# Kernel tuning notes

Hardware: AMD Instinct MI355X
Metric: run time of the kernel (lower is better)

The kernel has to match this reference:

```python
import jax, jax.numpy as jnp
import numpy as np

B, L, D = 64, 1024, 1024
NUM_CLASS = 126
C = NUM_CLASS + 2           # total tags incl. START/STOP
START, STOP = C - 2, C - 1


def setup_inputs() -> dict:
    key = jax.random.key(0)
    kx, kl, kw, kt, ky = jax.random.split(key, 5)
    x = jax.random.normal(kx, (B, L, D), dtype=jnp.float32)
    lengths = jax.random.randint(kl, (B,), L // 2, L + 1)
    mask = jnp.arange(L)[None, :] < lengths[:, None]          # prefix bool mask [B,L]
    y = jax.random.randint(ky, (B, L), 0, NUM_CLASS)
    W = jax.random.normal(kw, (D, C), dtype=jnp.float32) * 0.02
    b = jnp.zeros((C,), dtype=jnp.float32)
    transitions = jax.random.normal(kt, (C, C), dtype=jnp.float32)
    transitions = transitions.at[START, :].set(-1.0)
    transitions = transitions.at[:, STOP].set(-1.0)
    return {"x": x, "mask": mask, "y": y, "W": W, "b": b, "transitions": transitions}


def reference(x, mask, y, W, b, transitions):
    # fc (dropout is identity at eval time)
    emis = x @ W + b                                  # [B,L,C]
    seq_len = mask.sum(-1)                            # [B]

    # ---- Viterbi forward scan over time ----
    def step(scores, inp):
        e_l, m_l = inp                                # [B,C], [B]
        ns = scores[:, :, None] + transitions[None]   # [B,C_prev,C_cur]
        bp = jnp.argmax(ns, axis=1)                   # [B,C]
        new = jnp.max(ns, axis=1) + e_l
        scores = jnp.where(m_l[:, None], new, scores)
        return scores, bp

    scores0 = jnp.zeros((x.shape[0], C), dtype=emis.dtype)
    final, bps = jax.lax.scan(step, scores0, (emis.transpose(1, 0, 2), mask.T))
    final = final + transitions[:, STOP][None, :]
    last_tag = jnp.argmax(final, axis=-1)             # [B]

    # ---- vectorized backtracking (reverse scan) ----
    def bstep(cur, inp):
        bp_l, l = inp                                 # [B,C], scalar
        emit = jnp.where(l <= seq_len - 1, cur, 0)    # pad with 0 past seq end
        prev = jnp.take_along_axis(bp_l, cur[:, None], axis=1)[:, 0]
        upd = (l >= 1) & (l <= seq_len - 1)
        return jnp.where(upd, prev, cur), emit

    ls = jnp.arange(L - 1, -1, -1)
    _, path_rev = jax.lax.scan(bstep, last_tag, (bps[::-1], ls))
    best_paths = path_rev[::-1].T                     # [B,L] int
    return best_paths
```

## Files before the change

### kernel.cpp

```cpp
#include <hip/hip_runtime.h>
#include <stdint.h>

#define BB 64
#define LL 1024
#define DD 1024
#define CC 128
#define STOPTAG 127

__global__ __launch_bounds__(256) void k_emis(const float* __restrict__ x,
                                              const float* __restrict__ W,
                                              const float* __restrict__ bias,
                                              float* __restrict__ emis) {
    __shared__ float a_t[32][132];
    const int tid = threadIdx.x;
    const int bm  = blockIdx.x;
    const float* A = x + (size_t)bm * 128 * DD;
    const int tx = tid & 15, ty = tid >> 4;
    const int r0 = ty * 8, c0 = tx * 8;

    float acc[8][8];
#pragma unroll
    for (int i = 0; i < 8; ++i)
#pragma unroll
        for (int j = 0; j < 8; ++j) acc[i][j] = 0.0f;

    for (int kc = 0; kc < 32; ++kc) {
        __syncthreads();
#pragma unroll
        for (int i = 0; i < 4; ++i) {
            int s   = tid + 256 * i;
            int row = s >> 3;
            int k0  = (s & 7) * 4;
            float4 v = *(const float4*)(A + (size_t)row * DD + kc * 32 + k0);
            a_t[k0 + 0][row] = v.x;
            a_t[k0 + 1][row] = v.y;
            a_t[k0 + 2][row] = v.z;
            a_t[k0 + 3][row] = v.w;
        }
        __syncthreads();
        const float* Wp = W + (size_t)kc * 32 * CC;
#pragma unroll
        for (int k = 0; k < 32; ++k) {
            float4 w0 = *(const float4*)(Wp + k * CC + c0);
            float4 w1 = *(const float4*)(Wp + k * CC + c0 + 4);
            float4 pa = *(const float4*)&a_t[k][r0];
            float4 pb = *(const float4*)&a_t[k][r0 + 4];
            float av[8] = {pa.x, pa.y, pa.z, pa.w, pb.x, pb.y, pb.z, pb.w};
            float wv[8] = {w0.x, w0.y, w0.z, w0.w, w1.x, w1.y, w1.z, w1.w};
#pragma unroll
            for (int i = 0; i < 8; ++i)
#pragma unroll
                for (int j = 0; j < 8; ++j)
                    acc[i][j] = fmaf(av[i], wv[j], acc[i][j]);
        }
    }
    float4 bv0 = *(const float4*)(bias + c0);
    float4 bv1 = *(const float4*)(bias + c0 + 4);
    float bb[8] = {bv0.x, bv0.y, bv0.z, bv0.w, bv1.x, bv1.y, bv1.z, bv1.w};
#pragma unroll
    for (int i = 0; i < 8; ++i) {
        size_t row = (size_t)bm * 128 + r0 + i;
        float4 o0 = make_float4(acc[i][0] + bb[0], acc[i][1] + bb[1],
                                acc[i][2] + bb[2], acc[i][3] + bb[3]);
        float4 o1 = make_float4(acc[i][4] + bb[4], acc[i][5] + bb[5],
                                acc[i][6] + bb[6], acc[i][7] + bb[7]);
        *(float4*)(emis + row * CC + c0)     = o0;
        *(float4*)(emis + row * CC + c0 + 4) = o1;
    }
}


__global__ __launch_bounds__(512) void k_forward(float* __restrict__ emis,
                                                 const unsigned char* __restrict__ mask,
                                                 const float* __restrict__ T) {
    const int b    = blockIdx.x;
    const int tid  = threadIdx.x;
    const int w    = tid >> 6;
    const int lane = tid & 63;

    __shared__ float part[2][8][CC];
    __shared__ int s_len;
    if (tid == 0) s_len = 0;
    __syncthreads();

    if (tid < 256) {
        const bool is_b8 = (mask[1] != 0);
        int c;
        if (is_b8) {
            const uchar4* m4 = (const uchar4*)(mask + (size_t)b * LL);
            uchar4 mv = m4[tid];
            c = (mv.x != 0) + (mv.y != 0) + (mv.z != 0) + (mv.w != 0);
        } else {
            const int4* m4 = (const int4*)((const int*)(const void*)mask + (size_t)b * LL);
            int4 mv = m4[tid];
            c = (mv.x != 0) + (mv.y != 0) + (mv.z != 0) + (mv.w != 0);
        }
        atomicAdd(&s_len, c);
    }
    __syncthreads();
    const int len = s_len;

    float t0[16], t1[16];
#pragma unroll
    for (int j = 0; j < 16; ++j) {
        t0[j] = T[(size_t)(w * 16 + j) * CC + lane];
        t1[j] = T[(size_t)(w * 16 + j) * CC + lane + 64];
    }

    const int cc_fin = w * 16 + (lane & 15);
    float* eb = emis + (size_t)b * LL * CC;

    float s_val = 0.0f;
    float e_cur = eb[cc_fin];
    float e_n1  = eb[CC + cc_fin];

    for (int l = 0; l < len; ++l) {
        int lp = l + 2 < len ? l + 2 : len - 1;
        float e_n2 = eb[(size_t)lp * CC + cc_fin];

        float acc0 = -INFINITY, acc1 = -INFINITY;
#pragma unroll
        for (int jj = 0; jj < 8; ++jj) {
            float sa = __int_as_float(__builtin_amdgcn_readlane(__float_as_int(s_val), 2 * jj));
            float sb = __int_as_float(__builtin_amdgcn_readlane(__float_as_int(s_val), 2 * jj + 1));
            acc0 = fmaxf(fmaxf(sa + t0[2 * jj], sb + t0[2 * jj + 1]), acc0);
            acc1 = fmaxf(fmaxf(sa + t1[2 * jj], sb + t1[2 * jj + 1]), acc1);
        }
        int p = l & 1;
        part[p][w][lane]      = acc0;
        part[p][w][lane + 64] = acc1;
        asm volatile("s_waitcnt lgkmcnt(0)" ::: "memory");
        __builtin_amdgcn_s_barrier();
        float m0 = fmaxf(part[p][0][cc_fin], part[p][1][cc_fin]);
        float m1 = fmaxf(part[p][2][cc_fin], part[p][3][cc_fin]);
        float m2 = fmaxf(part[p][4][cc_fin], part[p][5][cc_fin]);
        float m3 = fmaxf(part[p][6][cc_fin], part[p][7][cc_fin]);
        float mx = fmaxf(fmaxf(m0, m1), fmaxf(m2, m3));
        s_val = mx + e_cur;
        eb[(size_t)l * CC + cc_fin] = s_val;
        e_cur = e_n1;
        e_n1  = e_n2;
    }
}

__device__ __forceinline__ unsigned mono_u32(float f) {
    unsigned u = __float_as_uint(f);
    return u ^ (unsigned)(((int)u >> 31) | 0x80000000);
}

__device__ __forceinline__ unsigned dpp_max64(unsigned m) {
    unsigned t;
    t = (unsigned)__builtin_amdgcn_update_dpp(0, (int)m, 0x111, 0xF, 0xF, true); m = m > t ? m : t;
    t = (unsigned)__builtin_amdgcn_update_dpp(0, (int)m, 0x112, 0xF, 0xF, true); m = m > t ? m : t;
    t = (unsigned)__builtin_amdgcn_update_dpp(0, (int)m, 0x114, 0xF, 0xF, true); m = m > t ? m : t;
    t = (unsigned)__builtin_amdgcn_update_dpp(0, (int)m, 0x118, 0xF, 0xF, true); m = m > t ? m : t;
    t = (unsigned)__builtin_amdgcn_update_dpp(0, (int)m, 0x142, 0xF, 0xF, true); m = m > t ? m : t;
    t = (unsigned)__builtin_amdgcn_update_dpp(0, (int)m, 0x143, 0xF, 0xF, true); m = m > t ? m : t;
    return m;
}

__device__ __forceinline__ int astep(float sA, float sB, int row,
                                     const float* ldsT, int lane) {
    int q = (row & 7) << 2;
    float c0 = sA + ldsT[row * CC + (lane ^ q)];
    float c1 = sB + ldsT[row * CC + ((lane ^ q) + 64)];
    unsigned m0 = mono_u32(c0), m1 = mono_u32(c1);
    unsigned m = m0 > m1 ? m0 : m1;
    m = dpp_max64(m);
    unsigned mx = (unsigned)__builtin_amdgcn_readlane((int)m, 63);
    unsigned long long bl0 = __ballot(m0 == mx);
    unsigned long long bl1 = __ballot(m1 == mx);
    return bl0 ? __builtin_ctzll(bl0) : (64 + __builtin_ctzll(bl1));
}

__global__ __launch_bounds__(64) void k_back(const float* __restrict__ slog,
                                             const unsigned char* __restrict__ mask,
                                             const float* __restrict__ T,
                                             int* __restrict__ out) {
    const int b    = blockIdx.x;
    const int lane = threadIdx.x;
    __shared__ float ldsT[CC * CC];

    {
        int q = (lane & 7) << 2;
        for (int r = 0; r < CC; ++r) {
            float v0 = T[(size_t)r * CC + lane];
            float v1 = T[(size_t)r * CC + lane + 64];
            ldsT[lane * CC + (r ^ q)]        = v0;
            ldsT[(lane + 64) * CC + (r ^ q)] = v1;
        }
    }
    int len = 0;
    {
        const bool is_b8 = (mask[1] != 0);
        if (is_b8) {
            const unsigned char* mrow = mask + (size_t)b * LL;
            for (int i = 0; i < 16; ++i)
                len += (int)__popcll(__ballot(mrow[lane + i * 64] != 0));
        } else {
            const int* mrow = (const int*)(const void*)mask + (size_t)b * LL;
            for (int i = 0; i < 16; ++i)
                len += (int)__popcll(__ballot(mrow[lane + i * 64] != 0));
        }
    }
    __syncthreads();

    const float* sb = slog + (size_t)b * LL * CC;
    int* ob         = out + (size_t)b * LL;

    for (int l = len + lane; l < LL; l += 64) ob[l] = 0;

    float f0 = sb[(size_t)(len - 1) * CC + lane];
    float f1 = sb[(size_t)(len - 1) * CC + lane + 64];
    int cur = astep(f0, f1, STOPTAG, ldsT, lane);
    if (lane == 0) ob[len - 1] = cur;

    int r = len - 2;
    float a0 = sb[(size_t)r * CC + lane];
    float a1 = sb[(size_t)r * CC + lane + 64];
    float b0 = sb[(size_t)(r - 1) * CC + lane];
    float b1 = sb[(size_t)(r - 1) * CC + lane + 64];
    while (r >= 2) {
        int rc = r - 2;
        int rd = r - 3 >= 0 ? r - 3 : 0;
        float n0 = sb[(size_t)rc * CC + lane];
        float n1 = sb[(size_t)rc * CC + lane + 64];
        float p0 = sb[(size_t)rd * CC + lane];
        float p1 = sb[(size_t)rd * CC + lane + 64];
        cur = astep(a0, a1, cur, ldsT, lane);
        if (lane == 0) ob[r] = cur;
        cur = astep(b0, b1, cur, ldsT, lane);
        if (lane == 0) ob[r - 1] = cur;
        a0 = n0; a1 = n1; b0 = p0; b1 = p1;
        r -= 2;
    }
    if (r == 1) {
        cur = astep(a0, a1, cur, ldsT, lane);
        if (lane == 0) ob[1] = cur;
        cur = astep(b0, b1, cur, ldsT, lane);
        if (lane == 0) ob[0] = cur;
    } else if (r == 0) {
        cur = astep(a0, a1, cur, ldsT, lane);
        if (lane == 0) ob[0] = cur;
    }
}

extern "C" void kernel_launch(void* const* d_in, const int* in_sizes, int n_in,
                              void* d_out, int out_size, void* d_ws, size_t ws_size,
                              hipStream_t stream) {
    (void)in_sizes; (void)n_in; (void)out_size; (void)ws_size;
    const float* x    = (const float*)d_in[0];
    const unsigned char* mask = (const unsigned char*)d_in[1];
    const float* W    = (const float*)d_in[3];
    const float* bias = (const float*)d_in[4];
    const float* T    = (const float*)d_in[5];
    int* out = (int*)d_out;

    float* emis = (float*)d_ws;

    k_emis<<<dim3(512), dim3(256), 0, stream>>>(x, W, bias, emis);
    k_forward<<<dim3(BB), dim3(512), 0, stream>>>(emis, mask, T);
    k_back<<<dim3(BB), dim3(64), 0, stream>>>(emis, mask, T, out);
}
```

Before: 1.296 ms.

## Stage emissions and scores through LDS in 16-step chunks in Viterbi forward

The forward scan now prefetches emission rows into double-buffered LDS chunks of 16 timesteps using coalesced float4 loads. Scores are buffered in LDS and written back to global memory a chunk at a time, replacing the per-step scalar global loads and stores. The partial-max buffer is transposed so each thread reads its 8 wave partials as two float4 LDS loads. The cost is extra LDS use and an extra barrier every 16 steps, and the chunk bookkeeping near the sequence end is intricate.

```diff
diff --git a/kernel.cpp b/kernel.cpp
--- a/kernel.cpp
+++ b/kernel.cpp
@@ -69,7 +69,6 @@
     }
 }
 
-
 __global__ __launch_bounds__(512) void k_forward(float* __restrict__ emis,
                                                  const unsigned char* __restrict__ mask,
                                                  const float* __restrict__ T) {
@@ -77,8 +76,12 @@
     const int tid  = threadIdx.x;
     const int w    = tid >> 6;
     const int lane = tid & 63;
-
-    __shared__ float part[2][8][CC];
+    const int trow = tid >> 5;
+    const int tcol = (tid & 31) * 4;
+
+    __shared__ __align__(16) float part[2][CC][12];
+    __shared__ __align__(16) float ldsE[2][16][CC];
+    __shared__ __align__(16) float ldsS[2][16][CC];
     __shared__ int s_len;
     if (tid == 0) s_len = 0;
     __syncthreads();
@@ -110,13 +113,31 @@
     const int cc_fin = w * 16 + (lane & 15);
     float* eb = emis + (size_t)b * LL * CC;
 
+    float4 rs;
+    {
+        float4 c0v = *(const float4*)(eb + (size_t)trow * CC + tcol);
+        float4 c1v = *(const float4*)(eb + (size_t)(16 + trow) * CC + tcol);
+        *(float4*)&ldsE[0][trow][tcol] = c0v;
+        *(float4*)&ldsE[1][trow][tcol] = c1v;
+        rs = *(const float4*)(eb + (size_t)(32 + trow) * CC + tcol);
+    }
+    __syncthreads();
+
     float s_val = 0.0f;
-    float e_cur = eb[cc_fin];
-    float e_n1  = eb[CC + cc_fin];
 
     for (int l = 0; l < len; ++l) {
-        int lp = l + 2 < len ? l + 2 : len - 1;
-        float e_n2 = eb[(size_t)lp * CC + cc_fin];
+        if ((l & 15) == 0 && l > 0) {
+            const int c = l >> 4;
+            asm volatile("s_waitcnt lgkmcnt(0)" ::: "memory");
+            __builtin_amdgcn_s_barrier();
+            asm volatile("" ::: "memory");
+            float4 v = *(const float4*)&ldsS[(c - 1) & 1][trow][tcol];
+            *(float4*)(eb + (size_t)(16 * (c - 1) + trow) * CC + tcol) = v;
+            *(float4*)&ldsE[(c + 1) & 1][trow][tcol] = rs;
+            int g = 16 * (c + 2) + trow;
+            g = g < len ? g : len - 1;
+            rs = *(const float4*)(eb + (size_t)g * CC + tcol);
+        }
 
         float acc0 = -INFINITY, acc1 = -INFINITY;
 #pragma unroll
@@ -126,20 +147,29 @@
             acc0 = fmaxf(fmaxf(sa + t0[2 * jj], sb + t0[2 * jj + 1]), acc0);
             acc1 = fmaxf(fmaxf(sa + t1[2 * jj], sb + t1[2 * jj + 1]), acc1);
         }
-        int p = l & 1;
-        part[p][w][lane]      = acc0;
-        part[p][w][lane + 64] = acc1;
+        const int p = l & 1;
+        part[p][lane][w]      = acc0;
+        part[p][lane + 64][w] = acc1;
         asm volatile("s_waitcnt lgkmcnt(0)" ::: "memory");
         __builtin_amdgcn_s_barrier();
-        float m0 = fmaxf(part[p][0][cc_fin], part[p][1][cc_fin]);
-        float m1 = fmaxf(part[p][2][cc_fin], part[p][3][cc_fin]);
-        float m2 = fmaxf(part[p][4][cc_fin], part[p][5][cc_fin]);
-        float m3 = fmaxf(part[p][6][cc_fin], part[p][7][cc_fin]);
-        float mx = fmaxf(fmaxf(m0, m1), fmaxf(m2, m3));
-        s_val = mx + e_cur;
-        eb[(size_t)l * CC + cc_fin] = s_val;
-        e_cur = e_n1;
-        e_n1  = e_n2;
+        asm volatile("" ::: "memory");
+
+        float4 q0 = *(const float4*)&part[p][cc_fin][0];
+        float4 q1 = *(const float4*)&part[p][cc_fin][4];
+        float m01 = fmaxf(q0.x, q0.y), m23 = fmaxf(q0.z, q0.w);
+        float m45 = fmaxf(q1.x, q1.y), m67 = fmaxf(q1.z, q1.w);
+        float mx  = fmaxf(fmaxf(m01, m23), fmaxf(m45, m67));
+        s_val = mx + ldsE[(l >> 4) & 1][l & 15][cc_fin];
+        if (lane < 16) ldsS[(l >> 4) & 1][l & 15][cc_fin] = s_val;
+    }
+
+    asm volatile("s_waitcnt lgkmcnt(0)" ::: "memory");
+    __syncthreads();
+    {
+        const int cf = (len - 1) >> 4;
+        float4 v = *(const float4*)&ldsS[cf & 1][trow][tcol];
+        int g = 16 * cf + trow;
+        if (g < len) *(float4*)(eb + (size_t)g * CC + tcol) = v;
     }
 }
 
```

After: 1.345 ms. 1.04x slower.

## Double-buffer emission GEMM LDS tiles and deepen backtrack prefetch pipeline

Applied to the files above, without the earlier changes.

The emission GEMM now uses two LDS buffers and prefetches the next K-chunk of x into registers while computing on the current one, cutting one barrier per iteration. The backtrack kernel issues loads for the first seven score rows before staging the transition matrix into LDS, and keeps a deeper rolling prefetch of rows ahead of the serial argmax chain. Both aim to hide global memory latency, at the cost of more registers and LDS in the GEMM. Reads at indices len-5 to len-7 are not clamped the way later prefetches are, which could read out of bounds for very short sequences.

```diff
diff --git a/kernel.cpp b/kernel.cpp
--- a/kernel.cpp
+++ b/kernel.cpp
@@ -11,7 +11,7 @@
                                               const float* __restrict__ W,
                                               const float* __restrict__ bias,
                                               float* __restrict__ emis) {
-    __shared__ float a_t[32][132];
+    __shared__ float a_t[2][32][132];
     const int tid = threadIdx.x;
     const int bm  = blockIdx.x;
     const float* A = x + (size_t)bm * 128 * DD;
@@ -24,27 +24,38 @@
 #pragma unroll
         for (int j = 0; j < 8; ++j) acc[i][j] = 0.0f;
 
+    float4 rs[4];
+#pragma unroll
+    for (int i = 0; i < 4; ++i) {
+        int s = tid + 256 * i, row = s >> 3, k0 = (s & 7) * 4;
+        rs[i] = *(const float4*)(A + (size_t)row * DD + k0);
+    }
+#pragma unroll
+    for (int i = 0; i < 4; ++i) {
+        int s = tid + 256 * i, row = s >> 3, k0 = (s & 7) * 4;
+        a_t[0][k0 + 0][row] = rs[i].x;
+        a_t[0][k0 + 1][row] = rs[i].y;
+        a_t[0][k0 + 2][row] = rs[i].z;
+        a_t[0][k0 + 3][row] = rs[i].w;
+    }
+    __syncthreads();
+
     for (int kc = 0; kc < 32; ++kc) {
-        __syncthreads();
-#pragma unroll
-        for (int i = 0; i < 4; ++i) {
-            int s   = tid + 256 * i;
-            int row = s >> 3;
-            int k0  = (s & 7) * 4;
-            float4 v = *(const float4*)(A + (size_t)row * DD + kc * 32 + k0);
-            a_t[k0 + 0][row] = v.x;
-            a_t[k0 + 1][row] = v.y;
-            a_t[k0 + 2][row] = v.z;
-            a_t[k0 + 3][row] = v.w;
-        }
-        __syncthreads();
+        if (kc + 1 < 32) {
+#pragma unroll
+            for (int i = 0; i < 4; ++i) {
+                int s = tid + 256 * i, row = s >> 3, k0 = (s & 7) * 4;
+                rs[i] = *(const float4*)(A + (size_t)row * DD + (kc + 1) * 32 + k0);
+            }
+        }
         const float* Wp = W + (size_t)kc * 32 * CC;
+        const float (*at)[132] = a_t[kc & 1];
 #pragma unroll
         for (int k = 0; k < 32; ++k) {
             float4 w0 = *(const float4*)(Wp + k * CC + c0);
             float4 w1 = *(const float4*)(Wp + k * CC + c0 + 4);
-            float4 pa = *(const float4*)&a_t[k][r0];
-            float4 pb = *(const float4*)&a_t[k][r0 + 4];
+            float4 pa = *(const float4*)&at[k][r0];
+            float4 pb = *(const float4*)&at[k][r0 + 4];
             float av[8] = {pa.x, pa.y, pa.z, pa.w, pb.x, pb.y, pb.z, pb.w};
             float wv[8] = {w0.x, w0.y, w0.z, w0.w, w1.x, w1.y, w1.z, w1.w};
 #pragma unroll
@@ -52,6 +63,18 @@
 #pragma unroll
                 for (int j = 0; j < 8; ++j)
                     acc[i][j] = fmaf(av[i], wv[j], acc[i][j]);
+        }
+        if (kc + 1 < 32) {
+#pragma unroll
+            for (int i = 0; i < 4; ++i) {
+                int s = tid + 256 * i, row = s >> 3, k0 = (s & 7) * 4;
+                a_t[(kc + 1) & 1][k0 + 0][row] = rs[i].x;
+                a_t[(kc + 1) & 1][k0 + 1][row] = rs[i].y;
+                a_t[(kc + 1) & 1][k0 + 2][row] = rs[i].z;
+                a_t[(kc + 1) & 1][k0 + 3][row] = rs[i].w;
+            }
+            asm volatile("s_waitcnt lgkmcnt(0)" ::: "memory");
+            __builtin_amdgcn_s_barrier();
         }
     }
     float4 bv0 = *(const float4*)(bias + c0);
@@ -181,15 +204,6 @@
     const int lane = threadIdx.x;
     __shared__ float ldsT[CC * CC];
 
-    {
-        int q = (lane & 7) << 2;
-        for (int r = 0; r < CC; ++r) {
-            float v0 = T[(size_t)r * CC + lane];
-            float v1 = T[(size_t)r * CC + lane + 64];
-            ldsT[lane * CC + (r ^ q)]        = v0;
-            ldsT[(lane + 64) * CC + (r ^ q)] = v1;
-        }
-    }
     int len = 0;
     {
         const bool is_b8 = (mask[1] != 0);
@@ -203,44 +217,64 @@
                 len += (int)__popcll(__ballot(mrow[lane + i * 64] != 0));
         }
     }
-    __syncthreads();
 
     const float* sb = slog + (size_t)b * LL * CC;
     int* ob         = out + (size_t)b * LL;
 
-    for (int l = len + lane; l < LL; l += 64) ob[l] = 0;
-
     float f0 = sb[(size_t)(len - 1) * CC + lane];
     float f1 = sb[(size_t)(len - 1) * CC + lane + 64];
+    float A0 = sb[(size_t)(len - 2) * CC + lane];
+    float A1 = sb[(size_t)(len - 2) * CC + lane + 64];
+    float B0 = sb[(size_t)(len - 3) * CC + lane];
+    float B1 = sb[(size_t)(len - 3) * CC + lane + 64];
+    float C0 = sb[(size_t)(len - 4) * CC + lane];
+    float C1 = sb[(size_t)(len - 4) * CC + lane + 64];
+    float D0 = sb[(size_t)(len - 5) * CC + lane];
+    float D1 = sb[(size_t)(len - 5) * CC + lane + 64];
+    float E0 = sb[(size_t)(len - 6) * CC + lane];
+    float E1 = sb[(size_t)(len - 6) * CC + lane + 64];
+    float F0 = sb[(size_t)(len - 7) * CC + lane];
+    float F1 = sb[(size_t)(len - 7) * CC + lane + 64];
+
+    {
+        int q = (lane & 7) << 2;
+        for (int r = 0; r < CC; ++r) {
+            float v0 = T[(size_t)r * CC + lane];
+            float v1 = T[(size_t)r * CC + lane + 64];
+            ldsT[lane * CC + (r ^ q)]        = v0;
+            ldsT[(lane + 64) * CC + (r ^ q)] = v1;
+        }
+    }
+    __syncthreads();
+
+    for (int l = len + lane; l < LL; l += 64) ob[l] = 0;
+
     int cur = astep(f0, f1, STOPTAG, ldsT, lane);
     if (lane == 0) ob[len - 1] = cur;
 
     int r = len - 2;
-    float a0 = sb[(size_t)r * CC + lane];
-    float a1 = sb[(size_t)r * CC + lane + 64];
-    float b0 = sb[(size_t)(r - 1) * CC + lane];
-    float b1 = sb[(size_t)(r - 1) * CC + lane + 64];
     while (r >= 2) {
-        int rc = r - 2;
-        int rd = r - 3 >= 0 ? r - 3 : 0;
-        float n0 = sb[(size_t)rc * CC + lane];
-        float n1 = sb[(size_t)rc * CC + lane + 64];
-        float p0 = sb[(size_t)rd * CC + lane];
-        float p1 = sb[(size_t)rd * CC + lane + 64];
-        cur = astep(a0, a1, cur, ldsT, lane);
+        cur = astep(A0, A1, cur, ldsT, lane);
         if (lane == 0) ob[r] = cur;
-        cur = astep(b0, b1, cur, ldsT, lane);
+        cur = astep(B0, B1, cur, ldsT, lane);
         if (lane == 0) ob[r - 1] = cur;
-        a0 = n0; a1 = n1; b0 = p0; b1 = p1;
+        A0 = C0; A1 = C1; B0 = D0; B1 = D1;
+        C0 = E0; C1 = E1; D0 = F0; D1 = F1;
+        int g0 = r - 6 >= 0 ? r - 6 : 0;
+        int g1 = r - 7 >= 0 ? r - 7 : 0;
+        E0 = sb[(size_t)g0 * CC + lane];
+        E1 = sb[(size_t)g0 * CC + lane + 64];
+        F0 = sb[(size_t)g1 * CC + lane];
+        F1 = sb[(size_t)g1 * CC + lane + 64];
         r -= 2;
     }
     if (r == 1) {
-        cur = astep(a0, a1, cur, ldsT, lane);
+        cur = astep(A0, A1, cur, ldsT, lane);
         if (lane == 0) ob[1] = cur;
-        cur = astep(b0, b1, cur, ldsT, lane);
+        cur = astep(B0, B1, cur, ldsT, lane);
         if (lane == 0) ob[0] = cur;
     } else if (r == 0) {
-        cur = astep(a0, a1, cur, ldsT, lane);
+        cur = astep(A0, A1, cur, ldsT, lane);
         if (lane == 0) ob[0] = cur;
     }
 }
```

Measured after the change: 2.005 ms. 1.55x slower.
